# Kernel tuning notes

Hardware: AMD Instinct MI355X
Metric: run time of the kernel (lower is better)

Reference implementation:

```python
import jax, jax.numpy as jnp
import numpy as np

NUM_HEADS = 16
HIDDEN = 1024
HEAD_DIM = HIDDEN // NUM_HEADS
B, L = 1, 2048


def setup_inputs() -> dict:
    key = jax.random.key(0)
    ks = jax.random.split(key, 5)
    scale = 1.0 / np.sqrt(HIDDEN)
    x = jax.random.normal(ks[0], (B, L, HIDDEN), dtype=jnp.float32)
    Wq = jax.random.normal(ks[1], (HIDDEN, HIDDEN), dtype=jnp.float32) * scale
    Wk = jax.random.normal(ks[2], (HIDDEN, HIDDEN), dtype=jnp.float32) * scale
    Wv = jax.random.normal(ks[3], (HIDDEN, HIDDEN), dtype=jnp.float32) * scale
    Wo = jax.random.normal(ks[4], (HIDDEN, HIDDEN), dtype=jnp.float32) * scale
    return {"x": x, "Wq": Wq, "Wk": Wk, "Wv": Wv, "Wo": Wo}


def reference(x, Wq, Wk, Wv, Wo):
    Bx, Lx, _ = x.shape
    # nn.Linear computes x @ W.T (bias=False)
    q = (x @ Wq.T).reshape(Bx, Lx, NUM_HEADS, HEAD_DIM)
    k = (x @ Wk.T).reshape(Bx, Lx, NUM_HEADS, HEAD_DIM)
    v = (x @ Wv.T).reshape(Bx, Lx, NUM_HEADS, HEAD_DIM)
    # elu(.)+1 feature map
    q = jax.nn.elu(q) + 1.0
    k = jax.nn.elu(k) + 1.0
    # causal linear-attention state via cumsum of kv outer products
    kv = jnp.einsum('blhd,blhe->blhde', k, v)           # [B,L,H,D,D]
    kv_cumsum = jnp.cumsum(kv, axis=1)
    k_cumsum = jnp.cumsum(k, axis=1)
    out = jnp.einsum('blhd,blhde->blhe', q, kv_cumsum)   # [B,L,H,D]
    denom = jnp.clip(jnp.einsum('blhd,blhd->blh', q, k_cumsum), 1e-6, None)
    out = out / denom[..., None]
    return out.reshape(Bx, Lx, HIDDEN) @ Wo.T
```

## Files before the change

### kernel.cpp

```cpp
#include <hip/hip_runtime.h>
#include <hip/hip_bf16.h>

typedef __attribute__((ext_vector_type(8))) short short8;
typedef __attribute__((ext_vector_type(4))) float floatx4;
typedef __attribute__((ext_vector_type(8))) unsigned short ushortx8;
typedef __attribute__((ext_vector_type(4))) unsigned short ushortx4;
typedef unsigned short u16;

#define HIDDEN 1024
#define NH 16
#define HD 64
#define SEQ 2048
#define CHUNK 128
#define NCHUNK (SEQ / CHUNK)

__device__ __forceinline__ u16 f2bf(float f) {
    union { float f; unsigned u; } v; v.f = f;
    unsigned r = v.u + 0x7fffu + ((v.u >> 16) & 1u);
    return (u16)(r >> 16);
}
__device__ __forceinline__ float bf2f(u16 u) {
    union { unsigned u; float f; } v; v.u = ((unsigned)u) << 16;
    return v.f;
}

__device__ __forceinline__ void gl_lds16(const u16* g, u16* l) {
    __builtin_amdgcn_global_load_lds(
        (const __attribute__((address_space(1))) void*)g,
        (__attribute__((address_space(3))) void*)l,
        16, 0, 0);
}

__global__ __launch_bounds__(256)
void convert_all(const float* __restrict__ x,  const float* __restrict__ Wq,
                 const float* __restrict__ Wk, const float* __restrict__ Wv,
                 const float* __restrict__ Wo,
                 u16* __restrict__ xb, u16* __restrict__ Wb, u16* __restrict__ Wob)
{
    const int total4 = 1572864;
    for (int idx = blockIdx.x * 256 + threadIdx.x; idx < total4; idx += gridDim.x * 256) {
        const float4* src; u16* dst; int off;
        if (idx < 524288)       { src = (const float4*)x;  dst = xb;            off = idx; }
        else if (idx < 786432)  { src = (const float4*)Wq; dst = Wb;            off = idx - 524288; }
        else if (idx < 1048576) { src = (const float4*)Wk; dst = Wb + 1048576;  off = idx - 786432; }
        else if (idx < 1310720) { src = (const float4*)Wv; dst = Wb + 2097152;  off = idx - 1048576; }
        else                    { src = (const float4*)Wo; dst = Wob;           off = idx - 1310720; }
        float4 v = src[off];
        ushortx4 u = { f2bf(v.x), f2bf(v.y), f2bf(v.z), f2bf(v.w) };
        *(ushortx4*)(dst + (size_t)off * 4) = u;
    }
}

__global__ __launch_bounds__(256, 3)
void qkv_gemm64(const u16* __restrict__ A, const u16* __restrict__ Bm,
                u16* __restrict__ qkb, u16* __restrict__ kT_b, u16* __restrict__ vT_b)
{
    __shared__ u16 As[64 * 64];
    __shared__ u16 Bs[128 * 64];
    const int n0 = blockIdx.x * 128, m0 = blockIdx.y * 64;
    const int t = threadIdx.x;
    const int lane = t & 63, wave = t >> 6;
    const int ln = lane & 15, q4 = lane >> 4;
    const int wm = (wave >> 1) * 32, wn = (wave & 1) * 64;
    const int r_in = t >> 3;
    const int csw = (((t & 7) ^ (r_in & 7)) << 3);

    const u16* Ag = A + (size_t)(m0 + r_in) * 1024 + csw;
    const u16* Bg = Bm + (size_t)(n0 + r_in) * 1024 + csw;

    floatx4 acc[2][4];
#pragma unroll
    for (int i = 0; i < 2; i++)
#pragma unroll
        for (int j = 0; j < 4; j++) acc[i][j] = (floatx4)0.0f;

    for (int k0 = 0; k0 < 1024; k0 += 64) {
        if (k0) __syncthreads();
        gl_lds16(Ag, &As[t * 8]);
        gl_lds16(Ag + 32 * 1024, &As[2048 + t * 8]);
#pragma unroll
        for (int i = 0; i < 4; i++)
            gl_lds16(Bg + (size_t)i * 32 * 1024, &Bs[i * 2048 + t * 8]);
        Ag += 64; Bg += 64;
        __syncthreads();
#pragma unroll
        for (int s = 0; s < 2; s++) {
            const int rc = (((s * 4 + q4) ^ (ln & 7)) << 3);
            short8 af[2], bfr[4];
#pragma unroll
            for (int i = 0; i < 2; i++)
                af[i] = *(const short8*)&As[(wm + i * 16 + ln) * 64 + rc];
#pragma unroll
            for (int j = 0; j < 4; j++)
                bfr[j] = *(const short8*)&Bs[(wn + j * 16 + ln) * 64 + rc];
#pragma unroll
            for (int i = 0; i < 2; i++)
#pragma unroll
                for (int j = 0; j < 4; j++)
                    acc[i][j] = __builtin_amdgcn_mfma_f32_16x16x32_bf16(af[i], bfr[j], acc[i][j], 0, 0, 0);
        }
    }
    const int grp = n0 >> 10;
#pragma unroll
    for (int i = 0; i < 2; i++)
#pragma unroll
        for (int j = 0; j < 4; j++) {
            const int mb = m0 + wm + i * 16 + q4 * 4;
            const int n = n0 + wn + j * 16 + ln;
            const int nh = n & 1023, h = nh >> 6, e = nh & 63;
            float vals[4];
#pragma unroll
            for (int r = 0; r < 4; r++) {
                float v = acc[i][j][r];
                if (grp < 2) v = (v > 0.f) ? (v + 1.f) : __expf(v);
                vals[r] = v;
            }
            if (grp == 0) {
#pragma unroll
                for (int r = 0; r < 4; r++) qkb[(size_t)(mb + r) * 2048 + nh] = f2bf(vals[r]);
            } else if (grp == 1) {
#pragma unroll
                for (int r = 0; r < 4; r++) qkb[(size_t)(mb + r) * 2048 + 1024 + nh] = f2bf(vals[r]);
                ushortx4 u = { f2bf(vals[0]), f2bf(vals[1]), f2bf(vals[2]), f2bf(vals[3]) };
                *(ushortx4*)&kT_b[(size_t)(h * 64 + e) * 2048 + mb] = u;
            } else {
                ushortx4 u = { f2bf(vals[0]), f2bf(vals[1]), f2bf(vals[2]), f2bf(vals[3]) };
                *(ushortx4*)&vT_b[(size_t)(h * 64 + e) * 2048 + mb] = u;
            }
        }
}

__global__ __launch_bounds__(256, 2)
void chunk_stats2(const u16* __restrict__ kT_b, const u16* __restrict__ vT_b,
                  float* __restrict__ S_ws, float* __restrict__ ksum_ws)
{
    __shared__ u16 kT_l[64 * 128];
    __shared__ u16 vT_l[64 * 128];
    const int c = blockIdx.x, h = blockIdx.y;
    const int t = threadIdx.x;
    const int lane = t & 63, w = t >> 6;
    const int ln = lane & 15, q4 = lane >> 4;
#pragma unroll
    for (int i = 0; i < 4; i++) {
        const int d0 = w * 16 + i * 4 + (lane >> 4);
        const int cc = lane & 15;
        const size_t gsrc = (size_t)(h * 64 + d0) * 2048 + c * 128 + ((cc ^ (d0 & 7)) << 3);
        gl_lds16(kT_b + gsrc, &kT_l[(w * 16 + i * 4) * 128 + lane * 8]);
        gl_lds16(vT_b + gsrc, &vT_l[(w * 16 + i * 4) * 128 + lane * 8]);
    }
    __syncthreads();
    floatx4 sacc[4];
#pragma unroll
    for (int j = 0; j < 4; j++) sacc[j] = (floatx4)0.0f;
#pragma unroll
    for (int ks = 0; ks < 4; ks++) {
        const int rc = (((ks * 4 + q4) ^ (ln & 7)) << 3);
        short8 af = *(const short8*)&kT_l[(w * 16 + ln) * 128 + rc];
#pragma unroll
        for (int j = 0; j < 4; j++) {
            short8 bfr = *(const short8*)&vT_l[(j * 16 + ln) * 128 + rc];
            sacc[j] = __builtin_amdgcn_mfma_f32_16x16x32_bf16(af, bfr, sacc[j], 0, 0, 0);
        }
    }
    float* Sp = S_ws + ((size_t)(h * NCHUNK + c) << 12);
#pragma unroll
    for (int j = 0; j < 4; j++)
#pragma unroll
        for (int r = 0; r < 4; r++) {
            int d = w * 16 + q4 * 4 + r;
            int e = j * 16 + ln;
            Sp[e * 64 + d] = sacc[j][r];
        }
    if (t < 64) {
        float s = 0.f;
#pragma unroll
        for (int cc = 0; cc < 16; cc++) {
            ushortx8 v8 = *(const ushortx8*)&kT_l[t * 128 + cc * 8];
#pragma unroll
            for (int jj = 0; jj < 8; jj++) s += bf2f(v8[jj]);
        }
        ksum_ws[(h * NCHUNK + c) * 64 + t] = s;
    }
}

__global__ __launch_bounds__(256)
void scan_kv(const float* __restrict__ S_ws, const float* __restrict__ ksum_ws,
             u16* __restrict__ kvpref_b, float* __restrict__ kspref)
{
    const int h = blockIdx.x, qt = blockIdx.y;
    const int t = threadIdx.x;
    const int li = qt * 1024 + t * 4;
    const int e = li >> 6, d0 = li & 63;
    const int slot = e * 64 + ((((d0 >> 3) ^ (e & 7)) << 3) | (d0 & 7));
    float a0 = 0.f, a1 = 0.f, a2 = 0.f, a3 = 0.f;
    for (int c = 0; c < 16; c++) {
        ushortx4 u = { f2bf(a0), f2bf(a1), f2bf(a2), f2bf(a3) };
        *(ushortx4*)&kvpref_b[(((size_t)(h * 16 + c)) << 12) + slot] = u;
        float4 s4 = *(const float4*)(S_ws + (((size_t)(h * 16 + c)) << 12) + li);
        a0 += s4.x; a1 += s4.y; a2 += s4.z; a3 += s4.w;
    }
    if (qt == 0 && t < 64) {
        float a = 0.f;
        for (int c = 0; c < 16; c++) {
            kspref[(h * 16 + c) * 64 + t] = a;
            a += ksum_ws[(h * 16 + c) * 64 + t];
        }
    }
}

__global__ __launch_bounds__(512, 2)
void attn_out2(const u16* __restrict__ qkb, const u16* __restrict__ vT_b,
               const u16* __restrict__ kvpref_b, const float* __restrict__ kspref,
               u16* __restrict__ attnb)
{
    __shared__ __align__(16) u16 smem[29824];
    u16* q_l   = smem;
    u16* k_l   = smem + 8192;
    u16* kvT_l = smem + 16384;
    u16* vT_l  = smem + 20480;
    u16* P_l   = smem;
    float* kpref  = (float*)(smem + 28672);
    float* denom4 = kpref + 64;

    const int c = blockIdx.x, h = blockIdx.y;
    const int t = threadIdx.x;
    const int lane = t & 63, w = t >> 6;
    const int ln = lane & 15, q4 = lane >> 4;

    {
        const int row = t >> 3, cc = t & 7;
        const size_t gq = (size_t)(c * CHUNK + row) * 2048 + h * 64
                        + (size_t)((cc ^ (row & 7)) << 3);
        gl_lds16(qkb + gq,        &q_l[t * 8]);
        gl_lds16(qkb + gq + 1024, &k_l[t * 8]);
        const int row2 = row + 64;
        const size_t gq2 = (size_t)(c * CHUNK + row2) * 2048 + h * 64
                         + (size_t)((cc ^ (row2 & 7)) << 3);
        gl_lds16(qkb + gq2,        &q_l[4096 + t * 8]);
        gl_lds16(qkb + gq2 + 1024, &k_l[4096 + t * 8]);
        const int d = t >> 4, cv = t & 15;
        gl_lds16(vT_b + (size_t)(h * 64 + d) * 2048 + c * 128 + ((cv ^ (d & 7)) << 3),
                 &vT_l[t * 8]);
        const int d2 = d + 32;
        gl_lds16(vT_b + (size_t)(h * 64 + d2) * 2048 + c * 128 + ((cv ^ (d2 & 7)) << 3),
                 &vT_l[4096 + t * 8]);
        gl_lds16(kvpref_b + (((size_t)(h * 16 + c)) << 12) + t * 8, &kvT_l[t * 8]);
    }
    if (t < 64) kpref[t] = kspref[(h * 16 + c) * 64 + t];
    __syncthreads();

    const int pm = (w >> 2) * 64, pn = (w & 3) * 32;
    floatx4 pacc[4][2];
#pragma unroll
    for (int i = 0; i < 4; i++)
#pragma unroll
        for (int j = 0; j < 2; j++) pacc[i][j] = (floatx4)0.0f;
#pragma unroll
    for (int s = 0; s < 2; s++) {
        const int rc = (((s * 4 + q4) ^ (ln & 7)) << 3);
        short8 af[4], bfr[2];
#pragma unroll
        for (int i = 0; i < 4; i++)
            af[i] = *(const short8*)&q_l[(pm + i * 16 + ln) * 64 + rc];
#pragma unroll
        for (int j = 0; j < 2; j++)
            bfr[j] = *(const short8*)&k_l[(pn + j * 16 + ln) * 64 + rc];
#pragma unroll
        for (int i = 0; i < 4; i++)
#pragma unroll
            for (int j = 0; j < 2; j++)
                pacc[i][j] = __builtin_amdgcn_mfma_f32_16x16x32_bf16(af[i], bfr[j], pacc[i][j], 0, 0, 0);
    }
#pragma unroll
    for (int i = 0; i < 4; i++)
#pragma unroll
        for (int r = 0; r < 4; r++) {
            int rowi = pm + i * 16 + q4 * 4 + r;
            float rs = 0.f;
#pragma unroll
            for (int j = 0; j < 2; j++) {
                int col = pn + j * 16 + ln;
                float p = pacc[i][j][r];
                if (col > rowi) p = 0.f;
                pacc[i][j][r] = p;
                rs += p;
            }
#pragma unroll
            for (int off = 1; off < 16; off <<= 1) rs += __shfl_xor(rs, off, 64);
            if (ln == 0) denom4[(w & 3) * 128 + rowi] = rs;
        }
    const int ob = w * 16;
    floatx4 oacc[4];
#pragma unroll
    for (int j = 0; j < 4; j++) oacc[j] = (floatx4)0.0f;
#pragma unroll
    for (int s = 0; s < 2; s++) {
        const int rc = (((s * 4 + q4) ^ (ln & 7)) << 3);
        short8 af = *(const short8*)&q_l[(ob + ln) * 64 + rc];
#pragma unroll
        for (int j = 0; j < 4; j++) {
            short8 bfr = *(const short8*)&kvT_l[(j * 16 + ln) * 64 + rc];
            oacc[j] = __builtin_amdgcn_mfma_f32_16x16x32_bf16(af, bfr, oacc[j], 0, 0, 0);
        }
    }
    __syncthreads();
    if (t < 128) {
        float s = 0.f;
#pragma unroll
        for (int c8 = 0; c8 < 8; c8++) {
            ushortx8 v8 = *(const ushortx8*)&q_l[t * 64 + ((c8 ^ (t & 7)) << 3)];
#pragma unroll
            for (int jj = 0; jj < 8; jj++) s += bf2f(v8[jj]) * kpref[c8 * 8 + jj];
        }
        denom4[t] += s;
    }
    __syncthreads();
#pragma unroll
    for (int i = 0; i < 4; i++)
#pragma unroll
        for (int j = 0; j < 2; j++)
#pragma unroll
            for (int r = 0; r < 4; r++) {
                int rowi = pm + i * 16 + q4 * 4 + r;
                int col = pn + j * 16 + ln;
                P_l[rowi * 136 + col] = f2bf(pacc[i][j][r]);
            }
    __syncthreads();
    for (int ks = 0; ks <= (w >> 1); ks++) {
        short8 af = *(const short8*)&P_l[(ob + ln) * 136 + ks * 32 + q4 * 8];
        const int rc = (((ks * 4 + q4) ^ (ln & 7)) << 3);
#pragma unroll
        for (int j = 0; j < 4; j++) {
            short8 bfr = *(const short8*)&vT_l[(j * 16 + ln) * 128 + rc];
            oacc[j] = __builtin_amdgcn_mfma_f32_16x16x32_bf16(af, bfr, oacc[j], 0, 0, 0);
        }
    }
#pragma unroll
    for (int r = 0; r < 4; r++) {
        const int rowi = ob + q4 * 4 + r;
        float den = denom4[rowi] + denom4[128 + rowi] + denom4[256 + rowi] + denom4[384 + rowi];
        den = fmaxf(den, 1e-6f);
#pragma unroll
        for (int j = 0; j < 4; j++) {
            int e = j * 16 + ln;
            attnb[(size_t)(c * CHUNK + rowi) * HIDDEN + h * HD + e] = f2bf(oacc[j][r] / den);
        }
    }
}

__global__ __launch_bounds__(256, 3)
void out_gemm64(const u16* __restrict__ A, const u16* __restrict__ Bm,
                float* __restrict__ out)
{
    __shared__ u16 As[64 * 64];
    __shared__ u16 Bs[64 * 64];
    const int n0 = blockIdx.x * 64, m0 = blockIdx.y * 64;
    const int t = threadIdx.x;
    const int lane = t & 63, wave = t >> 6;
    const int ln = lane & 15, q4 = lane >> 4;
    const int wm = (wave >> 1) * 32, wn = (wave & 1) * 32;
    const int r_in = t >> 3;
    const int csw = (((t & 7) ^ (r_in & 7)) << 3);

    const u16* Ag = A + (size_t)(m0 + r_in) * 1024 + csw;
    const u16* Bg = Bm + (size_t)(n0 + r_in) * 1024 + csw;

    floatx4 acc[2][2];
#pragma unroll
    for (int i = 0; i < 2; i++)
#pragma unroll
        for (int j = 0; j < 2; j++) acc[i][j] = (floatx4)0.0f;

    for (int k0 = 0; k0 < 1024; k0 += 64) {
        if (k0) __syncthreads();
        gl_lds16(Ag, &As[t * 8]);
        gl_lds16(Ag + 32 * 1024, &As[2048 + t * 8]);
        gl_lds16(Bg, &Bs[t * 8]);
        gl_lds16(Bg + 32 * 1024, &Bs[2048 + t * 8]);
        Ag += 64; Bg += 64;
        __syncthreads();
#pragma unroll
        for (int s = 0; s < 2; s++) {
            const int rc = (((s * 4 + q4) ^ (ln & 7)) << 3);
            short8 af[2], bfr[2];
#pragma unroll
            for (int i = 0; i < 2; i++)
                af[i] = *(const short8*)&As[(wm + i * 16 + ln) * 64 + rc];
#pragma unroll
            for (int j = 0; j < 2; j++)
                bfr[j] = *(const short8*)&Bs[(wn + j * 16 + ln) * 64 + rc];
#pragma unroll
            for (int i = 0; i < 2; i++)
#pragma unroll
                for (int j = 0; j < 2; j++)
                    acc[i][j] = __builtin_amdgcn_mfma_f32_16x16x32_bf16(af[i], bfr[j], acc[i][j], 0, 0, 0);
        }
    }
#pragma unroll
    for (int i = 0; i < 2; i++)
#pragma unroll
        for (int j = 0; j < 2; j++)
#pragma unroll
            for (int r = 0; r < 4; r++) {
                int m = m0 + wm + i * 16 + q4 * 4 + r;
                int n = n0 + wn + j * 16 + ln;
                out[(size_t)m * 1024 + n] = acc[i][j][r];
            }
}

extern "C" void kernel_launch(void* const* d_in, const int* in_sizes, int n_in,
                              void* d_out, int out_size, void* d_ws, size_t ws_size,
                              hipStream_t stream)
{
    const float* x  = (const float*)d_in[0];
    const float* Wq = (const float*)d_in[1];
    const float* Wk = (const float*)d_in[2];
    const float* Wv = (const float*)d_in[3];
    const float* Wo = (const float*)d_in[4];
    float* out = (float*)d_out;

    char* ws = (char*)d_ws;
    const size_t MB = 1024 * 1024;
    u16* xb    = (u16*)(ws);
    u16* Wb    = (u16*)(ws + 4 * MB);
    u16* Wob   = (u16*)(ws + 10 * MB);
    u16* qkb   = (u16*)(ws + 12 * MB);
    u16* kT_b  = (u16*)(ws + 20 * MB);
    u16* vT_b  = (u16*)(ws + 24 * MB);
    float* S_ws    = (float*)(ws + 28 * MB);
    float* ksum_ws = (float*)(ws + 32 * MB);
    u16* attnb = (u16*)(ws + 33 * MB);
    u16* kvpref_b = (u16*)(ws + 37 * MB);
    float* kspref = (float*)(ws + 39 * MB);

    convert_all<<<2048, 256, 0, stream>>>(x, Wq, Wk, Wv, Wo, xb, Wb, Wob);
    qkv_gemm64<<<dim3(24, 32), 256, 0, stream>>>(xb, Wb, qkb, kT_b, vT_b);
    chunk_stats2<<<dim3(NCHUNK, NH), 256, 0, stream>>>(kT_b, vT_b, S_ws, ksum_ws);
    scan_kv<<<dim3(NH, 4), 256, 0, stream>>>(S_ws, ksum_ws, kvpref_b, kspref);
    attn_out2<<<dim3(NCHUNK, NH), 512, 0, stream>>>(qkb, vT_b, kvpref_b, kspref, attnb);
    out_gemm64<<<dim3(16, 32), 256, 0, stream>>>(attnb, Wob, out);
}
```

Measured before the change: 123.7 us.

## Double-buffer LDS tiles in QKV and output GEMMs with async prefetch

Both GEMM kernels now keep two LDS buffers, prefetching the next K tile through direct global-to-LDS loads while MFMA compute runs on the current one. Explicit vmcnt waits and barriers replace the per-iteration full syncthreads pair, so loads of tile k+2 overlap compute of tile k. The cost is double the shared memory per block, which may lower occupancy under launch_bounds(256,3), and the correctness of the hand-written waitcnt counts.

```diff
diff --git a/kernel.cpp b/kernel.cpp
--- a/kernel.cpp
+++ b/kernel.cpp
@@ -55,8 +55,8 @@
 void qkv_gemm64(const u16* __restrict__ A, const u16* __restrict__ Bm,
                 u16* __restrict__ qkb, u16* __restrict__ kT_b, u16* __restrict__ vT_b)
 {
-    __shared__ u16 As[64 * 64];
-    __shared__ u16 Bs[128 * 64];
+    __shared__ u16 As[2][64 * 64];
+    __shared__ u16 Bs[2][128 * 64];
     const int n0 = blockIdx.x * 128, m0 = blockIdx.y * 64;
     const int t = threadIdx.x;
     const int lane = t & 63, wave = t >> 6;
@@ -74,32 +74,53 @@
 #pragma unroll
         for (int j = 0; j < 4; j++) acc[i][j] = (floatx4)0.0f;
 
-    for (int k0 = 0; k0 < 1024; k0 += 64) {
-        if (k0) __syncthreads();
-        gl_lds16(Ag, &As[t * 8]);
-        gl_lds16(Ag + 32 * 1024, &As[2048 + t * 8]);
+    auto stage = [&](int buf, int k) {
+        const int k0 = k * 64;
+        gl_lds16(Ag + k0, &As[buf][t * 8]);
+        gl_lds16(Ag + k0 + 32 * 1024, &As[buf][2048 + t * 8]);
 #pragma unroll
         for (int i = 0; i < 4; i++)
-            gl_lds16(Bg + (size_t)i * 32 * 1024, &Bs[i * 2048 + t * 8]);
-        Ag += 64; Bg += 64;
-        __syncthreads();
+            gl_lds16(Bg + k0 + (size_t)i * 32 * 1024, &Bs[buf][i * 2048 + t * 8]);
+    };
+    auto compute = [&](int buf) {
 #pragma unroll
         for (int s = 0; s < 2; s++) {
             const int rc = (((s * 4 + q4) ^ (ln & 7)) << 3);
             short8 af[2], bfr[4];
 #pragma unroll
             for (int i = 0; i < 2; i++)
-                af[i] = *(const short8*)&As[(wm + i * 16 + ln) * 64 + rc];
+                af[i] = *(const short8*)&As[buf][(wm + i * 16 + ln) * 64 + rc];
 #pragma unroll
             for (int j = 0; j < 4; j++)
-                bfr[j] = *(const short8*)&Bs[(wn + j * 16 + ln) * 64 + rc];
+                bfr[j] = *(const short8*)&Bs[buf][(wn + j * 16 + ln) * 64 + rc];
 #pragma unroll
             for (int i = 0; i < 2; i++)
 #pragma unroll
                 for (int j = 0; j < 4; j++)
                     acc[i][j] = __builtin_amdgcn_mfma_f32_16x16x32_bf16(af[i], bfr[j], acc[i][j], 0, 0, 0);
         }
-    }
+    };
+
+    stage(0, 0);
+    stage(1, 1);
+    for (int i = 0; i < 14; i++) {
+        asm volatile("s_waitcnt vmcnt(6)" ::: "memory");
+        __builtin_amdgcn_sched_barrier(0);
+        __builtin_amdgcn_s_barrier();
+        compute(i & 1);
+        __builtin_amdgcn_sched_barrier(0);
+        __builtin_amdgcn_s_barrier();
+        stage(i & 1, i + 2);
+    }
+    asm volatile("s_waitcnt vmcnt(6)" ::: "memory");
+    __builtin_amdgcn_sched_barrier(0);
+    __builtin_amdgcn_s_barrier();
+    compute(0);
+    asm volatile("s_waitcnt vmcnt(0)" ::: "memory");
+    __builtin_amdgcn_sched_barrier(0);
+    __builtin_amdgcn_s_barrier();
+    compute(1);
+
     const int grp = n0 >> 10;
 #pragma unroll
     for (int i = 0; i < 2; i++)
@@ -352,8 +373,8 @@
 void out_gemm64(const u16* __restrict__ A, const u16* __restrict__ Bm,
                 float* __restrict__ out)
 {
-    __shared__ u16 As[64 * 64];
-    __shared__ u16 Bs[64 * 64];
+    __shared__ u16 As[2][64 * 64];
+    __shared__ u16 Bs[2][64 * 64];
     const int n0 = blockIdx.x * 64, m0 = blockIdx.y * 64;
     const int t = threadIdx.x;
     const int lane = t & 63, wave = t >> 6;
@@ -371,31 +392,52 @@
 #pragma unroll
         for (int j = 0; j < 2; j++) acc[i][j] = (floatx4)0.0f;
 
-    for (int k0 = 0; k0 < 1024; k0 += 64) {
-        if (k0) __syncthreads();
-        gl_lds16(Ag, &As[t * 8]);
-        gl_lds16(Ag + 32 * 1024, &As[2048 + t * 8]);
-        gl_lds16(Bg, &Bs[t * 8]);
-        gl_lds16(Bg + 32 * 1024, &Bs[2048 + t * 8]);
-        Ag += 64; Bg += 64;
-        __syncthreads();
+    auto stage = [&](int buf, int k) {
+        const int k0 = k * 64;
+        gl_lds16(Ag + k0, &As[buf][t * 8]);
+        gl_lds16(Ag + k0 + 32 * 1024, &As[buf][2048 + t * 8]);
+        gl_lds16(Bg + k0, &Bs[buf][t * 8]);
+        gl_lds16(Bg + k0 + 32 * 1024, &Bs[buf][2048 + t * 8]);
+    };
+    auto compute = [&](int buf) {
 #pragma unroll
         for (int s = 0; s < 2; s++) {
             const int rc = (((s * 4 + q4) ^ (ln & 7)) << 3);
             short8 af[2], bfr[2];
 #pragma unroll
             for (int i = 0; i < 2; i++)
-                af[i] = *(const short8*)&As[(wm + i * 16 + ln) * 64 + rc];
+                af[i] = *(const short8*)&As[buf][(wm + i * 16 + ln) * 64 + rc];
 #pragma unroll
             for (int j = 0; j < 2; j++)
-                bfr[j] = *(const short8*)&Bs[(wn + j * 16 + ln) * 64 + rc];
+                bfr[j] = *(const short8*)&Bs[buf][(wn + j * 16 + ln) * 64 + rc];
 #pragma unroll
             for (int i = 0; i < 2; i++)
 #pragma unroll
                 for (int j = 0; j < 2; j++)
                     acc[i][j] = __builtin_amdgcn_mfma_f32_16x16x32_bf16(af[i], bfr[j], acc[i][j], 0, 0, 0);
         }
-    }
+    };
+
+    stage(0, 0);
+    stage(1, 1);
+    for (int i = 0; i < 14; i++) {
+        asm volatile("s_waitcnt vmcnt(4)" ::: "memory");
+        __builtin_amdgcn_sched_barrier(0);
+        __builtin_amdgcn_s_barrier();
+        compute(i & 1);
+        __builtin_amdgcn_sched_barrier(0);
+        __builtin_amdgcn_s_barrier();
+        stage(i & 1, i + 2);
+    }
+    asm volatile("s_waitcnt vmcnt(4)" ::: "memory");
+    __builtin_amdgcn_sched_barrier(0);
+    __builtin_amdgcn_s_barrier();
+    compute(0);
+    asm volatile("s_waitcnt vmcnt(0)" ::: "memory");
+    __builtin_amdgcn_sched_barrier(0);
+    __builtin_amdgcn_s_barrier();
+    compute(1);
+
 #pragma unroll
     for (int i = 0; i < 2; i++)
 #pragma unroll
```

Measured after the change: 124.2 us (median of 2 runs). No clear change (+0.5%).
